# Performance work log

Hardware: AMD Instinct MI355X
Metric: run time of the kernel (lower is better)

## Reference

```python
import jax, jax.numpy as jnp
import numpy as np

RMIN, RMAX = -5.0, 5.0
MIN_BIN, MIN_SLOPE = 1e-4, 1e-4
BATCH, DIM, NBINS, HID = 65536, 64, 8, 128
NLAYERS = 6
SPLIT = DIM // 2  # 32
PDIM = 3 * NBINS + 1  # 25


def _mlp(h, w1, c1, w2, c2, w3, c3, w4, c4):
    # equinox MLP, depth=3: relu on hidden layers, identity on output
    h = jax.nn.relu(h @ w1.T + c1)
    h = jax.nn.relu(h @ w2.T + c2)
    h = jax.nn.relu(h @ w3.T + c3)
    return h @ w4.T + c4


def _rqs_forward(x, params):
    # x: [B,T], params: [B,T,3K+1] -> (y, logdet) each [B,T]
    K = (params.shape[-1] - 1) // 3
    total = RMAX - RMIN
    widths = jax.nn.softmax(params[..., :K], axis=-1) * (total - K * MIN_BIN) + MIN_BIN
    heights = jax.nn.softmax(params[..., K:2 * K], axis=-1) * (total - K * MIN_BIN) + MIN_BIN
    slope_off = float(np.log(np.exp(1.0 - MIN_SLOPE) - 1.0))
    slopes = jax.nn.softplus(params[..., 2 * K:] + slope_off) + MIN_SLOPE  # [B,T,K+1]
    zero = jnp.zeros(widths.shape[:-1] + (1,), widths.dtype)
    x_pos = jnp.concatenate([zero, jnp.cumsum(widths, -1)], -1) + RMIN   # [B,T,K+1]
    y_pos = jnp.concatenate([zero, jnp.cumsum(heights, -1)], -1) + RMIN
    below, above = x < RMIN, x > RMAX
    sl, sr = slopes[..., 0], slopes[..., -1]
    y_lin_l = (x - RMIN) * sl + RMIN
    y_lin_r = (x - RMAX) * sr + RMAX
    # searchsorted(x_pos[1:-1], x, side='right') == count of knots <= x
    bin_idx = jnp.clip(jnp.sum(x_pos[..., 1:-1] <= x[..., None], axis=-1), 0, K - 1)
    take = lambda a, i: jnp.take_along_axis(a, i[..., None], axis=-1)[..., 0]
    x_k, x_k1 = take(x_pos, bin_idx), take(x_pos, bin_idx + 1)
    y_k, y_k1 = take(y_pos, bin_idx), take(y_pos, bin_idx + 1)
    d_k, d_k1 = take(slopes, bin_idx), take(slopes, bin_idx + 1)
    w, h = x_k1 - x_k, y_k1 - y_k
    xi = jnp.clip((x - x_k) / w, 0.0, 1.0)
    s = h / w
    xi1m = 1.0 - xi
    q = xi * xi1m
    num = s * xi * xi + d_k * q
    den = s + (d_k1 + d_k - 2.0 * s) * q
    y_sp = y_k + h * num / den
    deriv = s * s * (d_k1 * xi * xi + 2.0 * s * q + d_k * xi1m * xi1m) / (den * den)
    y = jnp.where(below, y_lin_l, jnp.where(above, y_lin_r, y_sp))
    ld = jnp.where(below, jnp.log(sl), jnp.where(above, jnp.log(sr), jnp.log(deriv)))
    return y, ld


def _coupling(x, w1, c1, w2, c2, w3, c3, w4, c4, midx, tidx):
    xm = x[:, midx]           # [B,32]
    xt = x[:, tidx]           # [B,32]
    params = _mlp(xm, w1, c1, w2, c2, w3, c3, w4, c4)  # [B, 32*25]
    params = params.reshape(xt.shape[0], xt.shape[1], PDIM)
    yt, ld = _rqs_forward(xt, params)
    y = jnp.zeros_like(x).at[:, midx].set(xm).at[:, tidx].set(yt)
    return y, jnp.sum(ld, axis=-1)


def _make_masks():
    half_m = np.arange(0, SPLIT, dtype=np.int32)          # mask==1 positions
    half_t = np.arange(SPLIT, DIM, dtype=np.int32)
    alt_m = np.arange(1, DIM, 2, dtype=np.int32)          # odd -> mask==1
    alt_t = np.arange(0, DIM, 2, dtype=np.int32)
    mi = np.stack([half_m if i % 2 == 0 else alt_m for i in range(NLAYERS)])
    ti = np.stack([half_t if i % 2 == 0 else alt_t for i in range(NLAYERS)])
    return jnp.asarray(mi), jnp.asarray(ti)


def setup_inputs() -> dict:
    key = jax.random.key(0)
    ks = jax.random.split(key, 10)
    sc = 0.05
    x = jax.random.normal(ks[0], (BATCH, DIM), jnp.float32)
    W1 = jax.random.normal(ks[1], (NLAYERS, HID, SPLIT), jnp.float32) * sc
    b1 = jax.random.normal(ks[2], (NLAYERS, HID), jnp.float32) * sc
    W2 = jax.random.normal(ks[3], (NLAYERS, HID, HID), jnp.float32) * sc
    b2 = jax.random.normal(ks[4], (NLAYERS, HID), jnp.float32) * sc
    W3 = jax.random.normal(ks[5], (NLAYERS, HID, HID), jnp.float32) * sc
    b3 = jax.random.normal(ks[6], (NLAYERS, HID), jnp.float32) * sc
    W4 = jax.random.normal(ks[7], (NLAYERS, SPLIT * PDIM, HID), jnp.float32) * sc
    b4 = jax.random.normal(ks[8], (NLAYERS, SPLIT * PDIM), jnp.float32) * sc
    mask_idx, transform_idx = _make_masks()
    return dict(x=x, W1=W1, b1=b1, W2=W2, b2=b2, W3=W3, b3=b3, W4=W4, b4=b4,
                mask_idx=mask_idx, transform_idx=transform_idx)


def reference(x, W1, b1, W2, b2, W3, b3, W4, b4, mask_idx, transform_idx):
    def step(carry, layer):
        xc, tot = carry
        w1, c1, w2, c2, w3, c3, w4, c4, mi, ti = layer
        y, ld = _coupling(xc, w1, c1, w2, c2, w3, c3, w4, c4, mi, ti)
        return (y, tot + ld), None
    init = (x, jnp.zeros(x.shape[0], x.dtype))
    (y, total_logdet), _ = jax.lax.scan(
        step, init, (W1, b1, W2, b2, W3, b3, W4, b4, mask_idx, transform_idx))
    return y, total_logdet
```

## Files before the change

kernel.cpp:

```cpp
#include <hip/hip_runtime.h>
#include <math.h>

#define BATCH   65536
#define DIM     64
#define HID     128
#define SPLIT   32
#define NBINS   8
#define PDIM    25
#define NLAYERS 6
#define R_MIN   (-5.0f)
#define R_MAX   (5.0f)
#define MIN_BIN   1.0e-4f
#define MIN_SLOPE 1.0e-4f
#define SOFF      0.54116666f

#define ROWSW 16
#define WAVES 4
#define MBLK  64
#define NT    256

#define N_W1  (HID*SPLIT)
#define N_W2  (HID*HID)
#define N_W4P (32*32*HID)
#define N_W4  (SPLIT*PDIM*HID)

typedef __attribute__((ext_vector_type(8))) short bf16x8;
typedef __attribute__((ext_vector_type(4))) float f32x4;

__device__ __forceinline__ short f2bf(float f) {
    unsigned u = __builtin_bit_cast(unsigned, f);
    unsigned r = u + 0x7FFFu + ((u >> 16) & 1u);
    return (short)(r >> 16);
}

__device__ __forceinline__ unsigned pk2(float a, float b) {
    unsigned r;
    asm("v_cvt_pk_bf16_f32 %0, %1, %2" : "=v"(r) : "v"(a), "v"(b));
    return r;
}

__device__ __forceinline__ bf16x8 ldfrag(const short* base) {
    short4 lo = *reinterpret_cast<const short4*>(base);
    short4 hi = *reinterpret_cast<const short4*>(base + 64);
    bf16x8 a;
    a[0]=lo.x; a[1]=lo.y; a[2]=lo.z; a[3]=lo.w;
    a[4]=hi.x; a[5]=hi.y; a[6]=hi.z; a[7]=hi.w;
    return a;
}

__global__ void cvt_weights(const float* __restrict__ W1, const float* __restrict__ W2,
                            const float* __restrict__ W3, const float* __restrict__ W4,
                            const float* __restrict__ b4,
                            short* __restrict__ o1, short* __restrict__ o2,
                            short* __restrict__ o3, short* __restrict__ o4,
                            float* __restrict__ b4q) {
    const int stride = gridDim.x * blockDim.x;
    const int i0 = blockIdx.x * blockDim.x + threadIdx.x;
    for (int i = i0; i < NLAYERS*N_W1; i += stride) {
        const int L = i >> 12, rem = i & 4095;
        const int nt = rem >> 9, q = rem & 511;
        const int l = q >> 3, e = q & 7;
        o1[i] = f2bf(W1[L*N_W1 + (nt*16 + (l&15))*SPLIT + (l>>4)*8 + e]);
    }
    for (int i = i0; i < NLAYERS*N_W2; i += stride) {
        const int L = i >> 14, rem = i & 16383;
        const int c = rem >> 9, q = rem & 511;
        const int nt = c >> 2, kt = c & 3;
        const int l = q >> 3, e = q & 7;
        const int src = L*N_W2 + (nt*16 + (l&15))*HID + kt*32 + (l>>4)*8 + e;
        o2[i] = f2bf(W2[src]);
        o3[i] = f2bf(W3[src]);
    }
    for (int i = i0; i < NLAYERS*N_W4P; i += stride) {
        const int L = i >> 17, rem = i & (N_W4P - 1);
        const int c = rem >> 9, q = rem & 511;
        const int tb = c >> 5, pq = (c >> 2) & 7, kt = c & 3;
        const int l = q >> 3, e = q & 7;
        const int t = tb*4 + ((l & 15) >> 2);
        const int p = pq*4 + (l & 3);
        o4[i] = (p < PDIM)
              ? f2bf(W4[(size_t)L*N_W4 + (size_t)(t*PDIM + p)*HID + kt*32 + (l>>4)*8 + e])
              : (short)0;
    }
    for (int i = i0; i < NLAYERS*SPLIT*32; i += stride) {
        const int L = i >> 10, rem = i & 1023;
        const int t = rem >> 5, p = rem & 31;
        b4q[i] = (p < PDIM) ? b4[L*SPLIT*PDIM + t*PDIM + p] : 0.0f;
    }
}

template<int UNR>
__global__ __launch_bounds__(NT, 4) void flow_layer(
    const float* xin, float* yout, float* logdet, const int first,
    const short* __restrict__ bW1, const float* __restrict__ b1,
    const short* __restrict__ bW2, const float* __restrict__ b2,
    const short* __restrict__ bW3, const float* __restrict__ b3,
    const short* __restrict__ bW4, const float* __restrict__ b4q,
    const int* __restrict__ mi, const int* __restrict__ ti)
{
    __shared__ short act[WAVES][32 * 64];
    __shared__ float xts[WAVES][ROWSW][33];

    const int tid = threadIdx.x;
    const int wv  = tid >> 6;
    const int l   = tid & 63;
    const int lr  = l & 15;
    const int lg  = l >> 4;
    const int rbase = blockIdx.x * MBLK + wv * ROWSW;

    short* const actw = &act[wv][0];

    {
        const int kcol = l & 31;
        const int mc = mi[kcol], tc = ti[kcol];
        const int r0 = l >> 5;
        #pragma unroll
        for (int it = 0; it < 8; ++it) {
            const int r = r0 + it * 2;
            const float* row = xin + (size_t)(rbase + r) * DIM;
            const float mv = row[mc];
            actw[(kcol >> 2)*64 + r*4 + (kcol & 3)] = f2bf(mv);
            xts[wv][r][kcol] = row[tc];
            if (first) yout[(size_t)(rbase + r) * DIM + mc] = mv;
        }
    }

    {
        const bf16x8 afr = ldfrag(&actw[(2*lg)*64 + lr*4]);
        f32x4 c[8];
        #pragma unroll
        for (int nt = 0; nt < 8; ++nt) {
            const float4 bv = *reinterpret_cast<const float4*>(b1 + nt*16 + lg*4);
            c[nt] = (f32x4){bv.x, bv.y, bv.z, bv.w};
        }
        #pragma unroll
        for (int nt = 0; nt < 8; ++nt) {
            const bf16x8 wfr = *reinterpret_cast<const bf16x8*>(bW1 + (size_t)nt*512 + l*8);
            c[nt] = __builtin_amdgcn_mfma_f32_16x16x32_bf16(wfr, afr, c[nt], 0, 0, 0);
        }
        #pragma unroll
        for (int nt = 0; nt < 8; ++nt) {
            const unsigned u0 = pk2(fmaxf(c[nt][0], 0.0f), fmaxf(c[nt][1], 0.0f));
            const unsigned u1 = pk2(fmaxf(c[nt][2], 0.0f), fmaxf(c[nt][3], 0.0f));
            *reinterpret_cast<uint2*>(&actw[(nt*4 + lg)*64 + lr*4]) = (uint2){u0, u1};
        }
    }

    #pragma unroll 1
    for (int ph = 0; ph < 2; ++ph) {
        const short* Wp = ph ? bW3 : bW2;
        const float* bp = ph ? b3  : b2;
        bf16x8 afr[4];
        #pragma unroll
        for (int kt = 0; kt < 4; ++kt)
            afr[kt] = ldfrag(&actw[(kt*8 + 2*lg)*64 + lr*4]);
        f32x4 c[8];
        #pragma unroll
        for (int nt = 0; nt < 8; ++nt) {
            const float4 bv = *reinterpret_cast<const float4*>(bp + nt*16 + lg*4);
            c[nt] = (f32x4){bv.x, bv.y, bv.z, bv.w};
        }
        #pragma unroll
        for (int kt = 0; kt < 4; ++kt)
            #pragma unroll
            for (int nt = 0; nt < 8; ++nt) {
                const bf16x8 wfr = *reinterpret_cast<const bf16x8*>(Wp + (size_t)(nt*4 + kt)*512 + l*8);
                c[nt] = __builtin_amdgcn_mfma_f32_16x16x32_bf16(wfr, afr[kt], c[nt], 0, 0, 0);
            }
        #pragma unroll
        for (int nt = 0; nt < 8; ++nt) {
            const unsigned u0 = pk2(fmaxf(c[nt][0], 0.0f), fmaxf(c[nt][1], 0.0f));
            const unsigned u1 = pk2(fmaxf(c[nt][2], 0.0f), fmaxf(c[nt][3], 0.0f));
            *reinterpret_cast<uint2*>(&actw[(nt*4 + lg)*64 + lr*4]) = (uint2){u0, u1};
        }
    }

    bf16x8 afr[4];
    #pragma unroll
    for (int kt = 0; kt < 4; ++kt)
        afr[kt] = ldfrag(&actw[(kt*8 + 2*lg)*64 + lr*4]);

    float ldacc = 0.0f;

    auto body = [&](const int tb) {
        const int t = tb*4 + lg;
        f32x4 c[7];
        #pragma unroll
        for (int pq = 0; pq < 7; ++pq) {
            const float4 bv = *reinterpret_cast<const float4*>(b4q + t*32 + pq*4);
            c[pq] = (f32x4){bv.x, bv.y, bv.z, bv.w};
        }
        #pragma unroll
        for (int kt = 0; kt < 4; ++kt)
            #pragma unroll
            for (int pq = 0; pq < 7; ++pq) {
                const bf16x8 wfr = *reinterpret_cast<const bf16x8*>(
                    bW4 + (size_t)((tb*8 + pq)*4 + kt)*512 + l*8);
                c[pq] = __builtin_amdgcn_mfma_f32_16x16x32_bf16(wfr, afr[kt], c[pq], 0, 0, 0);
            }

#define P(i) c[(i)>>2][(i)&3]
        float wd[NBINS], hg[NBINS];
        float sw = 0.0f, sh = 0.0f;
        #pragma unroll
        for (int i = 0; i < NBINS; ++i) { wd[i] = __expf(P(i));         sw += wd[i]; }
        #pragma unroll
        for (int i = 0; i < NBINS; ++i) { hg[i] = __expf(P(NBINS + i)); sh += hg[i]; }
        const float scw = __fdividef((R_MAX - R_MIN) - NBINS * MIN_BIN, sw);
        const float sch = __fdividef((R_MAX - R_MIN) - NBINS * MIN_BIN, sh);
        #pragma unroll
        for (int i = 0; i < NBINS; ++i) { wd[i] = wd[i]*scw + MIN_BIN; hg[i] = hg[i]*sch + MIN_BIN; }

        const float x = xts[wv][lr][t];

        float cx = R_MIN, cy = R_MIN;
        float x_k = R_MIN, y_k = R_MIN, wsel = wd[0], hsel = hg[0];
        float z0 = P(16), z1 = P(17);
        #pragma unroll
        for (int i = 1; i < NBINS; ++i) {
            cx += wd[i-1]; cy += hg[i-1];
            const bool tk = (cx <= x);
            x_k  = tk ? cx        : x_k;
            y_k  = tk ? cy        : y_k;
            wsel = tk ? wd[i]     : wsel;
            hsel = tk ? hg[i]     : hsel;
            z0   = tk ? P(16 + i) : z0;
            z1   = tk ? P(17 + i) : z1;
        }

        auto sp = [](float v) {
            const float z = v + SOFF;
            return ((z > 15.0f) ? z : __logf(1.0f + __expf(z))) + MIN_SLOPE;
        };
        const float d_k = sp(z0), d_k1 = sp(z1);
        const float sl0 = sp(P(16)), sl8 = sp(P(24));
#undef P

        const float invw = __fdividef(1.0f, wsel);
        float xi = (x - x_k) * invw;
        xi = fminf(fmaxf(xi, 0.0f), 1.0f);
        const float s    = hsel * invw;
        const float xi1m = 1.0f - xi;
        const float q    = xi * xi1m;
        const float num  = s * xi * xi + d_k * q;
        const float den  = s + (d_k1 + d_k - 2.0f * s) * q;
        const float invden = __fdividef(1.0f, den);
        const float y_sp = y_k + hsel * num * invden;
        const float deriv = s * s * (d_k1 * xi * xi + 2.0f * s * q + d_k * xi1m * xi1m)
                            * invden * invden;

        const bool below = x < R_MIN;
        const bool above = x > R_MAX;
        const float yv = below ? ((x - R_MIN) * sl0 + R_MIN)
                       : (above ? ((x - R_MAX) * sl8 + R_MAX) : y_sp);
        const float dv = below ? sl0 : (above ? sl8 : deriv);
        ldacc += __logf(dv);

        yout[(size_t)(rbase + lr) * DIM + ti[t]] = yv;
    };

    if constexpr (UNR == 1) {
        #pragma unroll 1
        for (int tb = 0; tb < 8; ++tb) body(tb);
    } else {
        #pragma unroll 1
        for (int tb = 0; tb < 8; tb += 2) { body(tb); body(tb + 1); }
    }

    ldacc += __shfl_xor(ldacc, 16, 64);
    ldacc += __shfl_xor(ldacc, 32, 64);
    if (l < 16) {
        const int row = rbase + lr;
        if (first) logdet[row] = ldacc;
        else       logdet[row] += ldacc;
    }
}

extern "C" void kernel_launch(void* const* d_in, const int* in_sizes, int n_in,
                              void* d_out, int out_size, void* d_ws, size_t ws_size,
                              hipStream_t stream) {
    const float* x  = (const float*)d_in[0];
    const float* W1 = (const float*)d_in[1];
    const float* b1 = (const float*)d_in[2];
    const float* W2 = (const float*)d_in[3];
    const float* b2 = (const float*)d_in[4];
    const float* W3 = (const float*)d_in[5];
    const float* b3 = (const float*)d_in[6];
    const float* W4 = (const float*)d_in[7];
    const float* b4 = (const float*)d_in[8];
    const int*   mi = (const int*)d_in[9];
    const int*   ti = (const int*)d_in[10];

    float* y      = (float*)d_out;
    float* logdet = y + (size_t)BATCH * DIM;

    short* bW1 = (short*)d_ws;
    short* bW2 = bW1 + NLAYERS * N_W1;
    short* bW3 = bW2 + NLAYERS * N_W2;
    short* bW4 = bW3 + NLAYERS * N_W2;
    float* b4q = (float*)(bW4 + (size_t)NLAYERS * N_W4P);

    cvt_weights<<<512, 256, 0, stream>>>(W1, W2, W3, W4, b4, bW1, bW2, bW3, bW4, b4q);

    dim3 grid(BATCH / MBLK), block(NT);
    for (int L = 0; L < NLAYERS; ++L) {
        const float* in = (L == 0) ? x : y;
        const int first = (L == 0) ? 1 : 0;
        const short* w1 = bW1 + (size_t)L * N_W1;
        const short* w2 = bW2 + (size_t)L * N_W2;
        const short* w3 = bW3 + (size_t)L * N_W2;
        const short* w4 = bW4 + (size_t)L * N_W4P;
        const float* bb1 = b1 + L * HID, *bb2 = b2 + L * HID, *bb3 = b3 + L * HID;
        const float* bq = b4q + (size_t)L * SPLIT * 32;
        const int* mil = mi + L * SPLIT, *til = ti + L * SPLIT;
        if (L == 0 || L == 1 || L == 4)
            flow_layer<1><<<grid, block, 0, stream>>>(in, y, logdet, first,
                w1, bb1, w2, bb2, w3, bb3, w4, bq, mil, til);
        else
            flow_layer<2><<<grid, block, 0, stream>>>(in, y, logdet, first,
                w1, bb1, w2, bb2, w3, bb3, w4, bq, mil, til);
    }
}
```

Baseline: 349.6 us.

## Fuse all six coupling layers into one kernel keeping rows in LDS

Replaces the six per-layer kernel launches with a single kernel that loads each wave's 16 rows of x once into padded shared memory. All layers then run with the row state held in LDS, and y is written back with vectorized stores at the end. This removes five launches and the global read/write round trips of y and logdet between layers. In exchange the LDS footprint grows, which may affect occupancy. The per-layer unroll-by-two specialization is also dropped, so every layer uses the single-step transform loop.

```diff
diff --git a/kernel.cpp b/kernel.cpp
--- a/kernel.cpp
+++ b/kernel.cpp
@@ -18,6 +18,7 @@
 #define WAVES 4
 #define MBLK  64
 #define NT    256
+#define XPAD  68
 
 #define N_W1  (HID*SPLIT)
 #define N_W2  (HID*HID)
@@ -89,17 +90,16 @@
     }
 }
 
-template<int UNR>
-__global__ __launch_bounds__(NT, 4) void flow_layer(
-    const float* xin, float* yout, float* logdet, const int first,
-    const short* __restrict__ bW1, const float* __restrict__ b1,
-    const short* __restrict__ bW2, const float* __restrict__ b2,
-    const short* __restrict__ bW3, const float* __restrict__ b3,
-    const short* __restrict__ bW4, const float* __restrict__ b4q,
-    const int* __restrict__ mi, const int* __restrict__ ti)
+__global__ __launch_bounds__(NT, 4) void flow_all(
+    const float* __restrict__ xin, float* __restrict__ yout, float* __restrict__ logdet,
+    const short* __restrict__ bW1, const float* __restrict__ b1a,
+    const short* __restrict__ bW2, const float* __restrict__ b2a,
+    const short* __restrict__ bW3, const float* __restrict__ b3a,
+    const short* __restrict__ bW4, const float* __restrict__ b4qa,
+    const int* __restrict__ mia, const int* __restrict__ tia)
 {
     __shared__ short act[WAVES][32 * 64];
-    __shared__ float xts[WAVES][ROWSW][33];
+    __shared__ float xf[WAVES][ROWSW][XPAD];
 
     const int tid = threadIdx.x;
     const int wv  = tid >> 6;
@@ -109,171 +109,187 @@
     const int rbase = blockIdx.x * MBLK + wv * ROWSW;
 
     short* const actw = &act[wv][0];
-
-    {
-        const int kcol = l & 31;
-        const int mc = mi[kcol], tc = ti[kcol];
-        const int r0 = l >> 5;
-        #pragma unroll
-        for (int it = 0; it < 8; ++it) {
-            const int r = r0 + it * 2;
-            const float* row = xin + (size_t)(rbase + r) * DIM;
-            const float mv = row[mc];
-            actw[(kcol >> 2)*64 + r*4 + (kcol & 3)] = f2bf(mv);
-            xts[wv][r][kcol] = row[tc];
-            if (first) yout[(size_t)(rbase + r) * DIM + mc] = mv;
+    float (* const xr)[XPAD] = xf[wv];
+
+    #pragma unroll
+    for (int i = 0; i < 4; ++i) {
+        const int r = (l >> 4) + i * 4;
+        const int d = (l & 15) * 4;
+        const float4 v = *reinterpret_cast<const float4*>(xin + (size_t)(rbase + r) * DIM + d);
+        *reinterpret_cast<float4*>(&xr[r][d]) = v;
+    }
+
+    float ldacc = 0.0f;
+
+    #pragma unroll 1
+    for (int L = 0; L < NLAYERS; ++L) {
+        const short* w1 = bW1 + (size_t)L * N_W1;
+        const short* w2 = bW2 + (size_t)L * N_W2;
+        const short* w3 = bW3 + (size_t)L * N_W2;
+        const short* w4 = bW4 + (size_t)L * N_W4P;
+        const float* bb1 = b1a + L * HID;
+        const float* bb2 = b2a + L * HID;
+        const float* bb3 = b3a + L * HID;
+        const float* bq  = b4qa + (size_t)L * SPLIT * 32;
+        const int* mil = mia + L * SPLIT;
+        const int* til = tia + L * SPLIT;
+
+        {
+            const int kcol = l & 31;
+            const int mc = mil[kcol];
+            const int r0 = l >> 5;
+            #pragma unroll
+            for (int it = 0; it < 8; ++it) {
+                const int r = r0 + it * 2;
+                actw[(kcol >> 2)*64 + r*4 + (kcol & 3)] = f2bf(xr[r][mc]);
+            }
         }
-    }
-
-    {
-        const bf16x8 afr = ldfrag(&actw[(2*lg)*64 + lr*4]);
-        f32x4 c[8];
-        #pragma unroll
-        for (int nt = 0; nt < 8; ++nt) {
-            const float4 bv = *reinterpret_cast<const float4*>(b1 + nt*16 + lg*4);
-            c[nt] = (f32x4){bv.x, bv.y, bv.z, bv.w};
+
+        {
+            const bf16x8 afr = ldfrag(&actw[(2*lg)*64 + lr*4]);
+            f32x4 c[8];
+            #pragma unroll
+            for (int nt = 0; nt < 8; ++nt) {
+                const float4 bv = *reinterpret_cast<const float4*>(bb1 + nt*16 + lg*4);
+                c[nt] = (f32x4){bv.x, bv.y, bv.z, bv.w};
+            }
+            #pragma unroll
+            for (int nt = 0; nt < 8; ++nt) {
+                const bf16x8 wfr = *reinterpret_cast<const bf16x8*>(w1 + (size_t)nt*512 + l*8);
+                c[nt] = __builtin_amdgcn_mfma_f32_16x16x32_bf16(wfr, afr, c[nt], 0, 0, 0);
+            }
+            #pragma unroll
+            for (int nt = 0; nt < 8; ++nt) {
+                const unsigned u0 = pk2(fmaxf(c[nt][0], 0.0f), fmaxf(c[nt][1], 0.0f));
+                const unsigned u1 = pk2(fmaxf(c[nt][2], 0.0f), fmaxf(c[nt][3], 0.0f));
+                *reinterpret_cast<uint2*>(&actw[(nt*4 + lg)*64 + lr*4]) = (uint2){u0, u1};
+            }
         }
-        #pragma unroll
-        for (int nt = 0; nt < 8; ++nt) {
-            const bf16x8 wfr = *reinterpret_cast<const bf16x8*>(bW1 + (size_t)nt*512 + l*8);
-            c[nt] = __builtin_amdgcn_mfma_f32_16x16x32_bf16(wfr, afr, c[nt], 0, 0, 0);
+
+        #pragma unroll 1
+        for (int ph = 0; ph < 2; ++ph) {
+            const short* Wp = ph ? w3 : w2;
+            const float* bp = ph ? bb3 : bb2;
+            bf16x8 afr[4];
+            #pragma unroll
+            for (int kt = 0; kt < 4; ++kt)
+                afr[kt] = ldfrag(&actw[(kt*8 + 2*lg)*64 + lr*4]);
+            f32x4 c[8];
+            #pragma unroll
+            for (int nt = 0; nt < 8; ++nt) {
+                const float4 bv = *reinterpret_cast<const float4*>(bp + nt*16 + lg*4);
+                c[nt] = (f32x4){bv.x, bv.y, bv.z, bv.w};
+            }
+            #pragma unroll
+            for (int kt = 0; kt < 4; ++kt)
+                #pragma unroll
+                for (int nt = 0; nt < 8; ++nt) {
+                    const bf16x8 wfr = *reinterpret_cast<const bf16x8*>(Wp + (size_t)(nt*4 + kt)*512 + l*8);
+                    c[nt] = __builtin_amdgcn_mfma_f32_16x16x32_bf16(wfr, afr[kt], c[nt], 0, 0, 0);
+                }
+            #pragma unroll
+            for (int nt = 0; nt < 8; ++nt) {
+                const unsigned u0 = pk2(fmaxf(c[nt][0], 0.0f), fmaxf(c[nt][1], 0.0f));
+                const unsigned u1 = pk2(fmaxf(c[nt][2], 0.0f), fmaxf(c[nt][3], 0.0f));
+                *reinterpret_cast<uint2*>(&actw[(nt*4 + lg)*64 + lr*4]) = (uint2){u0, u1};
+            }
         }
-        #pragma unroll
-        for (int nt = 0; nt < 8; ++nt) {
-            const unsigned u0 = pk2(fmaxf(c[nt][0], 0.0f), fmaxf(c[nt][1], 0.0f));
-            const unsigned u1 = pk2(fmaxf(c[nt][2], 0.0f), fmaxf(c[nt][3], 0.0f));
-            *reinterpret_cast<uint2*>(&actw[(nt*4 + lg)*64 + lr*4]) = (uint2){u0, u1};
-        }
-    }
-
-    #pragma unroll 1
-    for (int ph = 0; ph < 2; ++ph) {
-        const short* Wp = ph ? bW3 : bW2;
-        const float* bp = ph ? b3  : b2;
+
         bf16x8 afr[4];
         #pragma unroll
         for (int kt = 0; kt < 4; ++kt)
             afr[kt] = ldfrag(&actw[(kt*8 + 2*lg)*64 + lr*4]);
-        f32x4 c[8];
-        #pragma unroll
-        for (int nt = 0; nt < 8; ++nt) {
-            const float4 bv = *reinterpret_cast<const float4*>(bp + nt*16 + lg*4);
-            c[nt] = (f32x4){bv.x, bv.y, bv.z, bv.w};
+
+        #pragma unroll 1
+        for (int tb = 0; tb < 8; ++tb) {
+            const int t = tb*4 + lg;
+            f32x4 c[7];
+            #pragma unroll
+            for (int pq = 0; pq < 7; ++pq) {
+                const float4 bv = *reinterpret_cast<const float4*>(bq + t*32 + pq*4);
+                c[pq] = (f32x4){bv.x, bv.y, bv.z, bv.w};
+            }
+            #pragma unroll
+            for (int kt = 0; kt < 4; ++kt)
+                #pragma unroll
+                for (int pq = 0; pq < 7; ++pq) {
+                    const bf16x8 wfr = *reinterpret_cast<const bf16x8*>(
+                        w4 + (size_t)((tb*8 + pq)*4 + kt)*512 + l*8);
+                    c[pq] = __builtin_amdgcn_mfma_f32_16x16x32_bf16(wfr, afr[kt], c[pq], 0, 0, 0);
+                }
+
+#define P(i) c[(i)>>2][(i)&3]
+            float wd[NBINS], hg[NBINS];
+            float sw = 0.0f, sh = 0.0f;
+            #pragma unroll
+            for (int i = 0; i < NBINS; ++i) { wd[i] = __expf(P(i));         sw += wd[i]; }
+            #pragma unroll
+            for (int i = 0; i < NBINS; ++i) { hg[i] = __expf(P(NBINS + i)); sh += hg[i]; }
+            const float scw = __fdividef((R_MAX - R_MIN) - NBINS * MIN_BIN, sw);
+            const float sch = __fdividef((R_MAX - R_MIN) - NBINS * MIN_BIN, sh);
+            #pragma unroll
+            for (int i = 0; i < NBINS; ++i) { wd[i] = wd[i]*scw + MIN_BIN; hg[i] = hg[i]*sch + MIN_BIN; }
+
+            const int tdim = til[t];
+            const float x = xr[lr][tdim];
+
+            float cx = R_MIN, cy = R_MIN;
+            float x_k = R_MIN, y_k = R_MIN, wsel = wd[0], hsel = hg[0];
+            float z0 = P(16), z1 = P(17);
+            #pragma unroll
+            for (int i = 1; i < NBINS; ++i) {
+                cx += wd[i-1]; cy += hg[i-1];
+                const bool tk = (cx <= x);
+                x_k  = tk ? cx        : x_k;
+                y_k  = tk ? cy        : y_k;
+                wsel = tk ? wd[i]     : wsel;
+                hsel = tk ? hg[i]     : hsel;
+                z0   = tk ? P(16 + i) : z0;
+                z1   = tk ? P(17 + i) : z1;
+            }
+
+            auto sp = [](float v) {
+                const float z = v + SOFF;
+                return ((z > 15.0f) ? z : __logf(1.0f + __expf(z))) + MIN_SLOPE;
+            };
+            const float d_k = sp(z0), d_k1 = sp(z1);
+            const float sl0 = sp(P(16)), sl8 = sp(P(24));
+#undef P
+
+            const float invw = __fdividef(1.0f, wsel);
+            float xi = (x - x_k) * invw;
+            xi = fminf(fmaxf(xi, 0.0f), 1.0f);
+            const float s    = hsel * invw;
+            const float xi1m = 1.0f - xi;
+            const float q    = xi * xi1m;
+            const float num  = s * xi * xi + d_k * q;
+            const float den  = s + (d_k1 + d_k - 2.0f * s) * q;
+            const float invden = __fdividef(1.0f, den);
+            const float y_sp = y_k + hsel * num * invden;
+            const float deriv = s * s * (d_k1 * xi * xi + 2.0f * s * q + d_k * xi1m * xi1m)
+                                * invden * invden;
+
+            const bool below = x < R_MIN;
+            const bool above = x > R_MAX;
+            const float yv = below ? ((x - R_MIN) * sl0 + R_MIN)
+                           : (above ? ((x - R_MAX) * sl8 + R_MAX) : y_sp);
+            const float dv = below ? sl0 : (above ? sl8 : deriv);
+            ldacc += __logf(dv);
+
+            xr[lr][tdim] = yv;
         }
-        #pragma unroll
-        for (int kt = 0; kt < 4; ++kt)
-            #pragma unroll
-            for (int nt = 0; nt < 8; ++nt) {
-                const bf16x8 wfr = *reinterpret_cast<const bf16x8*>(Wp + (size_t)(nt*4 + kt)*512 + l*8);
-                c[nt] = __builtin_amdgcn_mfma_f32_16x16x32_bf16(wfr, afr[kt], c[nt], 0, 0, 0);
-            }
-        #pragma unroll
-        for (int nt = 0; nt < 8; ++nt) {
-            const unsigned u0 = pk2(fmaxf(c[nt][0], 0.0f), fmaxf(c[nt][1], 0.0f));
-            const unsigned u1 = pk2(fmaxf(c[nt][2], 0.0f), fmaxf(c[nt][3], 0.0f));
-            *reinterpret_cast<uint2*>(&actw[(nt*4 + lg)*64 + lr*4]) = (uint2){u0, u1};
-        }
-    }
-
-    bf16x8 afr[4];
+    }
+
     #pragma unroll
-    for (int kt = 0; kt < 4; ++kt)
-        afr[kt] = ldfrag(&actw[(kt*8 + 2*lg)*64 + lr*4]);
-
-    float ldacc = 0.0f;
-
-    auto body = [&](const int tb) {
-        const int t = tb*4 + lg;
-        f32x4 c[7];
-        #pragma unroll
-        for (int pq = 0; pq < 7; ++pq) {
-            const float4 bv = *reinterpret_cast<const float4*>(b4q + t*32 + pq*4);
-            c[pq] = (f32x4){bv.x, bv.y, bv.z, bv.w};
-        }
-        #pragma unroll
-        for (int kt = 0; kt < 4; ++kt)
-            #pragma unroll
-            for (int pq = 0; pq < 7; ++pq) {
-                const bf16x8 wfr = *reinterpret_cast<const bf16x8*>(
-                    bW4 + (size_t)((tb*8 + pq)*4 + kt)*512 + l*8);
-                c[pq] = __builtin_amdgcn_mfma_f32_16x16x32_bf16(wfr, afr[kt], c[pq], 0, 0, 0);
-            }
-
-#define P(i) c[(i)>>2][(i)&3]
-        float wd[NBINS], hg[NBINS];
-        float sw = 0.0f, sh = 0.0f;
-        #pragma unroll
-        for (int i = 0; i < NBINS; ++i) { wd[i] = __expf(P(i));         sw += wd[i]; }
-        #pragma unroll
-        for (int i = 0; i < NBINS; ++i) { hg[i] = __expf(P(NBINS + i)); sh += hg[i]; }
-        const float scw = __fdividef((R_MAX - R_MIN) - NBINS * MIN_BIN, sw);
-        const float sch = __fdividef((R_MAX - R_MIN) - NBINS * MIN_BIN, sh);
-        #pragma unroll
-        for (int i = 0; i < NBINS; ++i) { wd[i] = wd[i]*scw + MIN_BIN; hg[i] = hg[i]*sch + MIN_BIN; }
-
-        const float x = xts[wv][lr][t];
-
-        float cx = R_MIN, cy = R_MIN;
-        float x_k = R_MIN, y_k = R_MIN, wsel = wd[0], hsel = hg[0];
-        float z0 = P(16), z1 = P(17);
-        #pragma unroll
-        for (int i = 1; i < NBINS; ++i) {
-            cx += wd[i-1]; cy += hg[i-1];
-            const bool tk = (cx <= x);
-            x_k  = tk ? cx        : x_k;
-            y_k  = tk ? cy        : y_k;
-            wsel = tk ? wd[i]     : wsel;
-            hsel = tk ? hg[i]     : hsel;
-            z0   = tk ? P(16 + i) : z0;
-            z1   = tk ? P(17 + i) : z1;
-        }
-
-        auto sp = [](float v) {
-            const float z = v + SOFF;
-            return ((z > 15.0f) ? z : __logf(1.0f + __expf(z))) + MIN_SLOPE;
-        };
-        const float d_k = sp(z0), d_k1 = sp(z1);
-        const float sl0 = sp(P(16)), sl8 = sp(P(24));
-#undef P
-
-        const float invw = __fdividef(1.0f, wsel);
-        float xi = (x - x_k) * invw;
-        xi = fminf(fmaxf(xi, 0.0f), 1.0f);
-        const float s    = hsel * invw;
-        const float xi1m = 1.0f - xi;
-        const float q    = xi * xi1m;
-        const float num  = s * xi * xi + d_k * q;
-        const float den  = s + (d_k1 + d_k - 2.0f * s) * q;
-        const float invden = __fdividef(1.0f, den);
-        const float y_sp = y_k + hsel * num * invden;
-        const float deriv = s * s * (d_k1 * xi * xi + 2.0f * s * q + d_k * xi1m * xi1m)
-                            * invden * invden;
-
-        const bool below = x < R_MIN;
-        const bool above = x > R_MAX;
-        const float yv = below ? ((x - R_MIN) * sl0 + R_MIN)
-                       : (above ? ((x - R_MAX) * sl8 + R_MAX) : y_sp);
-        const float dv = below ? sl0 : (above ? sl8 : deriv);
-        ldacc += __logf(dv);
-
-        yout[(size_t)(rbase + lr) * DIM + ti[t]] = yv;
-    };
-
-    if constexpr (UNR == 1) {
-        #pragma unroll 1
-        for (int tb = 0; tb < 8; ++tb) body(tb);
-    } else {
-        #pragma unroll 1
-        for (int tb = 0; tb < 8; tb += 2) { body(tb); body(tb + 1); }
-    }
-
+    for (int i = 0; i < 4; ++i) {
+        const int r = (l >> 4) + i * 4;
+        const int d = (l & 15) * 4;
+        *reinterpret_cast<float4*>(yout + (size_t)(rbase + r) * DIM + d) =
+            *reinterpret_cast<const float4*>(&xr[r][d]);
+    }
     ldacc += __shfl_xor(ldacc, 16, 64);
     ldacc += __shfl_xor(ldacc, 32, 64);
-    if (l < 16) {
-        const int row = rbase + lr;
-        if (first) logdet[row] = ldacc;
-        else       logdet[row] += ldacc;
-    }
+    if (l < 16) logdet[rbase + lr] = ldacc;
 }
 
 extern "C" void kernel_launch(void* const* d_in, const int* in_sizes, int n_in,
@@ -303,21 +319,6 @@
     cvt_weights<<<512, 256, 0, stream>>>(W1, W2, W3, W4, b4, bW1, bW2, bW3, bW4, b4q);
 
     dim3 grid(BATCH / MBLK), block(NT);
-    for (int L = 0; L < NLAYERS; ++L) {
-        const float* in = (L == 0) ? x : y;
-        const int first = (L == 0) ? 1 : 0;
-        const short* w1 = bW1 + (size_t)L * N_W1;
-        const short* w2 = bW2 + (size_t)L * N_W2;
-        const short* w3 = bW3 + (size_t)L * N_W2;
-        const short* w4 = bW4 + (size_t)L * N_W4P;
-        const float* bb1 = b1 + L * HID, *bb2 = b2 + L * HID, *bb3 = b3 + L * HID;
-        const float* bq = b4q + (size_t)L * SPLIT * 32;
-        const int* mil = mi + L * SPLIT, *til = ti + L * SPLIT;
-        if (L == 0 || L == 1 || L == 4)
-            flow_layer<1><<<grid, block, 0, stream>>>(in, y, logdet, first,
-                w1, bb1, w2, bb2, w3, bb3, w4, bq, mil, til);
-        else
-            flow_layer<2><<<grid, block, 0, stream>>>(in, y, logdet, first,
-                w1, bb1, w2, bb2, w3, bb3, w4, bq, mil, til);
-    }
-}
+    flow_all<<<grid, block, 0, stream>>>(x, y, logdet,
+        bW1, b1, bW2, b2, bW3, b3, bW4, b4q, mi, ti);
+}
```

Result: slower. 481.0 us, median of 4 (+37.6%).

## Software-pipeline W4 MFMA of next tile with spline math of current tile

Applied to the files above, without the earlier changes.

Restructures the final-layer loop so the weight loads and MFMAs for the next group of transformed dimensions are interleaved with the scalar rational-quadratic spline computation of the current group, using two ping-pong accumulator sets. This is meant to hide global weight-load latency and keep the matrix units busy alongside the transcendental and VALU work. It also drops the per-layer UNR template variants in favour of one kernel and rebalances the softmax sums into a tree. The cost is higher register pressure from two live accumulator arrays plus a weight fragment buffer, which under launch_bounds(256,4) could cause spills.

```diff
diff --git a/kernel.cpp b/kernel.cpp
--- a/kernel.cpp
+++ b/kernel.cpp
@@ -89,7 +89,6 @@
     }
 }
 
-template<int UNR>
 __global__ __launch_bounds__(NT, 4) void flow_layer(
     const float* xin, float* yout, float* logdet, const int first,
     const short* __restrict__ bW1, const float* __restrict__ b1,
@@ -126,7 +125,7 @@
     }
 
     {
-        const bf16x8 afr = ldfrag(&actw[(2*lg)*64 + lr*4]);
+        const bf16x8 afr0 = ldfrag(&actw[(2*lg)*64 + lr*4]);
         f32x4 c[8];
         #pragma unroll
         for (int nt = 0; nt < 8; ++nt) {
@@ -136,7 +135,7 @@
         #pragma unroll
         for (int nt = 0; nt < 8; ++nt) {
             const bf16x8 wfr = *reinterpret_cast<const bf16x8*>(bW1 + (size_t)nt*512 + l*8);
-            c[nt] = __builtin_amdgcn_mfma_f32_16x16x32_bf16(wfr, afr, c[nt], 0, 0, 0);
+            c[nt] = __builtin_amdgcn_mfma_f32_16x16x32_bf16(wfr, afr0, c[nt], 0, 0, 0);
         }
         #pragma unroll
         for (int nt = 0; nt < 8; ++nt) {
@@ -182,59 +181,68 @@
 
     float ldacc = 0.0f;
 
-    auto body = [&](const int tb) {
+    auto loadgrp = [&](bf16x8* wfr, int tb, int kt) {
+        #pragma unroll
+        for (int pq = 0; pq < 7; ++pq)
+            wfr[pq] = *reinterpret_cast<const bf16x8*>(
+                bW4 + (size_t)((tb*8 + pq)*4 + kt)*512 + l*8);
+    };
+    auto mfmagrp = [&](f32x4* c, const bf16x8* wfr, int kt) {
+        #pragma unroll
+        for (int pq = 0; pq < 7; ++pq)
+            c[pq] = __builtin_amdgcn_mfma_f32_16x16x32_bf16(wfr[pq], afr[kt], c[pq], 0, 0, 0);
+    };
+    auto biasinit = [&](f32x4* c, int tb) {
         const int t = tb*4 + lg;
-        f32x4 c[7];
         #pragma unroll
         for (int pq = 0; pq < 7; ++pq) {
             const float4 bv = *reinterpret_cast<const float4*>(b4q + t*32 + pq*4);
             c[pq] = (f32x4){bv.x, bv.y, bv.z, bv.w};
         }
-        #pragma unroll
-        for (int kt = 0; kt < 4; ++kt)
-            #pragma unroll
-            for (int pq = 0; pq < 7; ++pq) {
-                const bf16x8 wfr = *reinterpret_cast<const bf16x8*>(
-                    bW4 + (size_t)((tb*8 + pq)*4 + kt)*512 + l*8);
-                c[pq] = __builtin_amdgcn_mfma_f32_16x16x32_bf16(wfr, afr[kt], c[pq], 0, 0, 0);
-            }
-
-#define P(i) c[(i)>>2][(i)&3]
+    };
+
+    auto stage = [&](f32x4* cC, f32x4* cN, const int tb, const bool doNext) {
+        bf16x8 wfr[7];
+        if (doNext) { biasinit(cN, tb + 1); loadgrp(wfr, tb + 1, 0); }
+
         float wd[NBINS], hg[NBINS];
-        float sw = 0.0f, sh = 0.0f;
-        #pragma unroll
-        for (int i = 0; i < NBINS; ++i) { wd[i] = __expf(P(i));         sw += wd[i]; }
-        #pragma unroll
-        for (int i = 0; i < NBINS; ++i) { hg[i] = __expf(P(NBINS + i)); sh += hg[i]; }
+        #pragma unroll
+        for (int i = 0; i < NBINS; ++i) wd[i] = __expf(cC[i>>2][i&3]);
+        #pragma unroll
+        for (int i = 0; i < NBINS; ++i) hg[i] = __expf(cC[(NBINS+i)>>2][(NBINS+i)&3]);
+        const float sw = ((wd[0]+wd[1]) + (wd[2]+wd[3])) + ((wd[4]+wd[5]) + (wd[6]+wd[7]));
+        const float sh = ((hg[0]+hg[1]) + (hg[2]+hg[3])) + ((hg[4]+hg[5]) + (hg[6]+hg[7]));
         const float scw = __fdividef((R_MAX - R_MIN) - NBINS * MIN_BIN, sw);
         const float sch = __fdividef((R_MAX - R_MIN) - NBINS * MIN_BIN, sh);
         #pragma unroll
         for (int i = 0; i < NBINS; ++i) { wd[i] = wd[i]*scw + MIN_BIN; hg[i] = hg[i]*sch + MIN_BIN; }
 
-        const float x = xts[wv][lr][t];
-
+        if (doNext) { mfmagrp(cN, wfr, 0); loadgrp(wfr, tb + 1, 1); }
+
+        const float x = xts[wv][lr][tb*4 + lg];
         float cx = R_MIN, cy = R_MIN;
         float x_k = R_MIN, y_k = R_MIN, wsel = wd[0], hsel = hg[0];
-        float z0 = P(16), z1 = P(17);
+        float z0 = cC[4][0], z1 = cC[4][1];
         #pragma unroll
         for (int i = 1; i < NBINS; ++i) {
             cx += wd[i-1]; cy += hg[i-1];
             const bool tk = (cx <= x);
-            x_k  = tk ? cx        : x_k;
-            y_k  = tk ? cy        : y_k;
-            wsel = tk ? wd[i]     : wsel;
-            hsel = tk ? hg[i]     : hsel;
-            z0   = tk ? P(16 + i) : z0;
-            z1   = tk ? P(17 + i) : z1;
-        }
+            x_k  = tk ? cx : x_k;
+            y_k  = tk ? cy : y_k;
+            wsel = tk ? wd[i] : wsel;
+            hsel = tk ? hg[i] : hsel;
+            z0   = tk ? cC[(16+i)>>2][(16+i)&3] : z0;
+            z1   = tk ? cC[(17+i)>>2][(17+i)&3] : z1;
+        }
+
+        if (doNext) { mfmagrp(cN, wfr, 1); loadgrp(wfr, tb + 1, 2); }
 
         auto sp = [](float v) {
             const float z = v + SOFF;
             return ((z > 15.0f) ? z : __logf(1.0f + __expf(z))) + MIN_SLOPE;
         };
         const float d_k = sp(z0), d_k1 = sp(z1);
-        const float sl0 = sp(P(16)), sl8 = sp(P(24));
-#undef P
+        const float sl0 = sp(cC[4][0]), sl8 = sp(cC[6][0]);
 
         const float invw = __fdividef(1.0f, wsel);
         float xi = (x - x_k) * invw;
@@ -249,22 +257,30 @@
         const float deriv = s * s * (d_k1 * xi * xi + 2.0f * s * q + d_k * xi1m * xi1m)
                             * invden * invden;
 
+        if (doNext) { mfmagrp(cN, wfr, 2); loadgrp(wfr, tb + 1, 3); }
+
         const bool below = x < R_MIN;
         const bool above = x > R_MAX;
         const float yv = below ? ((x - R_MIN) * sl0 + R_MIN)
                        : (above ? ((x - R_MAX) * sl8 + R_MAX) : y_sp);
         const float dv = below ? sl0 : (above ? sl8 : deriv);
         ldacc += __logf(dv);
-
-        yout[(size_t)(rbase + lr) * DIM + ti[t]] = yv;
+        yout[(size_t)(rbase + lr) * DIM + ti[tb*4 + lg]] = yv;
+
+        if (doNext) { mfmagrp(cN, wfr, 3); }
     };
 
-    if constexpr (UNR == 1) {
-        #pragma unroll 1
-        for (int tb = 0; tb < 8; ++tb) body(tb);
-    } else {
-        #pragma unroll 1
-        for (int tb = 0; tb < 8; tb += 2) { body(tb); body(tb + 1); }
+    f32x4 cA[7], cB[7];
+    {
+        bf16x8 wfr[7];
+        biasinit(cA, 0);
+        #pragma unroll
+        for (int kt = 0; kt < 4; ++kt) { loadgrp(wfr, 0, kt); mfmagrp(cA, wfr, kt); }
+    }
+    #pragma unroll 1
+    for (int tb = 0; tb < 8; tb += 2) {
+        stage(cA, cB, tb,     true);
+        stage(cB, cA, tb + 1, tb + 1 < 7);
     }
 
     ldacc += __shfl_xor(ldacc, 16, 64);
@@ -304,20 +320,12 @@
 
     dim3 grid(BATCH / MBLK), block(NT);
     for (int L = 0; L < NLAYERS; ++L) {
-        const float* in = (L == 0) ? x : y;
-        const int first = (L == 0) ? 1 : 0;
-        const short* w1 = bW1 + (size_t)L * N_W1;
-        const short* w2 = bW2 + (size_t)L * N_W2;
-        const short* w3 = bW3 + (size_t)L * N_W2;
-        const short* w4 = bW4 + (size_t)L * N_W4P;
-        const float* bb1 = b1 + L * HID, *bb2 = b2 + L * HID, *bb3 = b3 + L * HID;
-        const float* bq = b4q + (size_t)L * SPLIT * 32;
-        const int* mil = mi + L * SPLIT, *til = ti + L * SPLIT;
-        if (L == 0 || L == 1 || L == 4)
-            flow_layer<1><<<grid, block, 0, stream>>>(in, y, logdet, first,
-                w1, bb1, w2, bb2, w3, bb3, w4, bq, mil, til);
-        else
-            flow_layer<2><<<grid, block, 0, stream>>>(in, y, logdet, first,
-                w1, bb1, w2, bb2, w3, bb3, w4, bq, mil, til);
-    }
-}
+        flow_layer<<<grid, block, 0, stream>>>(
+            (L == 0) ? x : y, y, logdet, (L == 0) ? 1 : 0,
+            bW1 + (size_t)L * N_W1, b1 + L * HID,
+            bW2 + (size_t)L * N_W2, b2 + L * HID,
+            bW3 + (size_t)L * N_W2, b3 + L * HID,
+            bW4 + (size_t)L * N_W4P, b4q + (size_t)L * SPLIT * 32,
+            mi + L * SPLIT, ti + L * SPLIT);
+    }
+}
```

Result: slower. 481.5 us (+37.7%).

## Split each 16-row tile's MLP output columns across two cooperating waves

Applied to the files above, without the earlier changes.

Blocks go from four independent waves on 64 rows to two waves sharing one 16-row tile. Each wave computes half of every layer's output columns, with barriers between layers on a shared activation buffer, and the two waves' logdet partials are combined through LDS. This halves the weight-fragment loads and accumulators per wave, lowering register pressure and shortening the per-row critical path so more waves can overlap. The cost is extra __syncthreads, twice as many waves reloading the same weights, and removal of the per-layer unroll-variant selection.

```diff
diff --git a/kernel.cpp b/kernel.cpp
--- a/kernel.cpp
+++ b/kernel.cpp
@@ -14,10 +14,8 @@
 #define MIN_SLOPE 1.0e-4f
 #define SOFF      0.54116666f
 
-#define ROWSW 16
-#define WAVES 4
-#define MBLK  64
-#define NT    256
+#define ROWSB 16
+#define NT    128
 
 #define N_W1  (HID*SPLIT)
 #define N_W2  (HID*HID)
@@ -89,8 +87,7 @@
     }
 }
 
-template<int UNR>
-__global__ __launch_bounds__(NT, 4) void flow_layer(
+__global__ __launch_bounds__(NT, 8) void flow_layer(
     const float* xin, float* yout, float* logdet, const int first,
     const short* __restrict__ bW1, const float* __restrict__ b1,
     const short* __restrict__ bW2, const float* __restrict__ b2,
@@ -98,53 +95,58 @@
     const short* __restrict__ bW4, const float* __restrict__ b4q,
     const int* __restrict__ mi, const int* __restrict__ ti)
 {
-    __shared__ short act[WAVES][32 * 64];
-    __shared__ float xts[WAVES][ROWSW][33];
+    __shared__ short act[32 * 64];
+    __shared__ float xts[ROWSB][33];
+    __shared__ float ldp[2][17];
 
     const int tid = threadIdx.x;
-    const int wv  = tid >> 6;
+    const int w   = tid >> 6;
     const int l   = tid & 63;
     const int lr  = l & 15;
     const int lg  = l >> 4;
-    const int rbase = blockIdx.x * MBLK + wv * ROWSW;
-
-    short* const actw = &act[wv][0];
+    const int rbase = blockIdx.x * ROWSB;
 
     {
-        const int kcol = l & 31;
+        const int kcol = tid & 31;
         const int mc = mi[kcol], tc = ti[kcol];
-        const int r0 = l >> 5;
-        #pragma unroll
-        for (int it = 0; it < 8; ++it) {
-            const int r = r0 + it * 2;
+        const int r0 = tid >> 5;
+        #pragma unroll
+        for (int it = 0; it < 4; ++it) {
+            const int r = r0 + it * 4;
             const float* row = xin + (size_t)(rbase + r) * DIM;
             const float mv = row[mc];
-            actw[(kcol >> 2)*64 + r*4 + (kcol & 3)] = f2bf(mv);
-            xts[wv][r][kcol] = row[tc];
+            act[(kcol >> 2)*64 + r*4 + (kcol & 3)] = f2bf(mv);
+            xts[r][kcol] = row[tc];
             if (first) yout[(size_t)(rbase + r) * DIM + mc] = mv;
         }
     }
+    __syncthreads();
 
     {
-        const bf16x8 afr = ldfrag(&actw[(2*lg)*64 + lr*4]);
-        f32x4 c[8];
-        #pragma unroll
-        for (int nt = 0; nt < 8; ++nt) {
+        const bf16x8 afr = ldfrag(&act[(2*lg)*64 + lr*4]);
+        f32x4 c[4];
+        #pragma unroll
+        for (int j = 0; j < 4; ++j) {
+            const int nt = w*4 + j;
             const float4 bv = *reinterpret_cast<const float4*>(b1 + nt*16 + lg*4);
-            c[nt] = (f32x4){bv.x, bv.y, bv.z, bv.w};
-        }
-        #pragma unroll
-        for (int nt = 0; nt < 8; ++nt) {
+            c[j] = (f32x4){bv.x, bv.y, bv.z, bv.w};
+        }
+        #pragma unroll
+        for (int j = 0; j < 4; ++j) {
+            const int nt = w*4 + j;
             const bf16x8 wfr = *reinterpret_cast<const bf16x8*>(bW1 + (size_t)nt*512 + l*8);
-            c[nt] = __builtin_amdgcn_mfma_f32_16x16x32_bf16(wfr, afr, c[nt], 0, 0, 0);
-        }
-        #pragma unroll
-        for (int nt = 0; nt < 8; ++nt) {
-            const unsigned u0 = pk2(fmaxf(c[nt][0], 0.0f), fmaxf(c[nt][1], 0.0f));
-            const unsigned u1 = pk2(fmaxf(c[nt][2], 0.0f), fmaxf(c[nt][3], 0.0f));
-            *reinterpret_cast<uint2*>(&actw[(nt*4 + lg)*64 + lr*4]) = (uint2){u0, u1};
-        }
-    }
+            c[j] = __builtin_amdgcn_mfma_f32_16x16x32_bf16(wfr, afr, c[j], 0, 0, 0);
+        }
+        __syncthreads();
+        #pragma unroll
+        for (int j = 0; j < 4; ++j) {
+            const int nt = w*4 + j;
+            const unsigned u0 = pk2(fmaxf(c[j][0], 0.0f), fmaxf(c[j][1], 0.0f));
+            const unsigned u1 = pk2(fmaxf(c[j][2], 0.0f), fmaxf(c[j][3], 0.0f));
+            *reinterpret_cast<uint2*>(&act[(nt*4 + lg)*64 + lr*4]) = (uint2){u0, u1};
+        }
+    }
+    __syncthreads();
 
     #pragma unroll 1
     for (int ph = 0; ph < 2; ++ph) {
@@ -153,36 +155,43 @@
         bf16x8 afr[4];
         #pragma unroll
         for (int kt = 0; kt < 4; ++kt)
-            afr[kt] = ldfrag(&actw[(kt*8 + 2*lg)*64 + lr*4]);
-        f32x4 c[8];
-        #pragma unroll
-        for (int nt = 0; nt < 8; ++nt) {
+            afr[kt] = ldfrag(&act[(kt*8 + 2*lg)*64 + lr*4]);
+        f32x4 c[4];
+        #pragma unroll
+        for (int j = 0; j < 4; ++j) {
+            const int nt = w*4 + j;
             const float4 bv = *reinterpret_cast<const float4*>(bp + nt*16 + lg*4);
-            c[nt] = (f32x4){bv.x, bv.y, bv.z, bv.w};
+            c[j] = (f32x4){bv.x, bv.y, bv.z, bv.w};
         }
         #pragma unroll
         for (int kt = 0; kt < 4; ++kt)
             #pragma unroll
-            for (int nt = 0; nt < 8; ++nt) {
+            for (int j = 0; j < 4; ++j) {
+                const int nt = w*4 + j;
                 const bf16x8 wfr = *reinterpret_cast<const bf16x8*>(Wp + (size_t)(nt*4 + kt)*512 + l*8);
-                c[nt] = __builtin_amdgcn_mfma_f32_16x16x32_bf16(wfr, afr[kt], c[nt], 0, 0, 0);
+                c[j] = __builtin_amdgcn_mfma_f32_16x16x32_bf16(wfr, afr[kt], c[j], 0, 0, 0);
             }
-        #pragma unroll
-        for (int nt = 0; nt < 8; ++nt) {
-            const unsigned u0 = pk2(fmaxf(c[nt][0], 0.0f), fmaxf(c[nt][1], 0.0f));
-            const unsigned u1 = pk2(fmaxf(c[nt][2], 0.0f), fmaxf(c[nt][3], 0.0f));
-            *reinterpret_cast<uint2*>(&actw[(nt*4 + lg)*64 + lr*4]) = (uint2){u0, u1};
-        }
+        __syncthreads();
+        #pragma unroll
+        for (int j = 0; j < 4; ++j) {
+            const int nt = w*4 + j;
+            const unsigned u0 = pk2(fmaxf(c[j][0], 0.0f), fmaxf(c[j][1], 0.0f));
+            const unsigned u1 = pk2(fmaxf(c[j][2], 0.0f), fmaxf(c[j][3], 0.0f));
+            *reinterpret_cast<uint2*>(&act[(nt*4 + lg)*64 + lr*4]) = (uint2){u0, u1};
+        }
+        __syncthreads();
     }
 
     bf16x8 afr[4];
     #pragma unroll
     for (int kt = 0; kt < 4; ++kt)
-        afr[kt] = ldfrag(&actw[(kt*8 + 2*lg)*64 + lr*4]);
+        afr[kt] = ldfrag(&act[(kt*8 + 2*lg)*64 + lr*4]);
 
     float ldacc = 0.0f;
 
-    auto body = [&](const int tb) {
+    #pragma unroll 1
+    for (int tbl = 0; tbl < 4; ++tbl) {
+        const int tb = w*4 + tbl;
         const int t = tb*4 + lg;
         f32x4 c[7];
         #pragma unroll
@@ -201,17 +210,18 @@
 
 #define P(i) c[(i)>>2][(i)&3]
         float wd[NBINS], hg[NBINS];
-        float sw = 0.0f, sh = 0.0f;
-        #pragma unroll
-        for (int i = 0; i < NBINS; ++i) { wd[i] = __expf(P(i));         sw += wd[i]; }
-        #pragma unroll
-        for (int i = 0; i < NBINS; ++i) { hg[i] = __expf(P(NBINS + i)); sh += hg[i]; }
+        #pragma unroll
+        for (int i = 0; i < NBINS; ++i) wd[i] = __expf(P(i));
+        #pragma unroll
+        for (int i = 0; i < NBINS; ++i) hg[i] = __expf(P(NBINS + i));
+        const float sw = ((wd[0]+wd[1]) + (wd[2]+wd[3])) + ((wd[4]+wd[5]) + (wd[6]+wd[7]));
+        const float sh = ((hg[0]+hg[1]) + (hg[2]+hg[3])) + ((hg[4]+hg[5]) + (hg[6]+hg[7]));
         const float scw = __fdividef((R_MAX - R_MIN) - NBINS * MIN_BIN, sw);
         const float sch = __fdividef((R_MAX - R_MIN) - NBINS * MIN_BIN, sh);
         #pragma unroll
         for (int i = 0; i < NBINS; ++i) { wd[i] = wd[i]*scw + MIN_BIN; hg[i] = hg[i]*sch + MIN_BIN; }
 
-        const float x = xts[wv][lr][t];
+        const float x = xts[lr][t];
 
         float cx = R_MIN, cy = R_MIN;
         float x_k = R_MIN, y_k = R_MIN, wsel = wd[0], hsel = hg[0];
@@ -220,10 +230,10 @@
         for (int i = 1; i < NBINS; ++i) {
             cx += wd[i-1]; cy += hg[i-1];
             const bool tk = (cx <= x);
-            x_k  = tk ? cx        : x_k;
-            y_k  = tk ? cy        : y_k;
-            wsel = tk ? wd[i]     : wsel;
-            hsel = tk ? hg[i]     : hsel;
+            x_k  = tk ? cx : x_k;
+            y_k  = tk ? cy : y_k;
+            wsel = tk ? wd[i] : wsel;
+            hsel = tk ? hg[i] : hsel;
             z0   = tk ? P(16 + i) : z0;
             z1   = tk ? P(17 + i) : z1;
         }
@@ -257,22 +267,17 @@
         ldacc += __logf(dv);
 
         yout[(size_t)(rbase + lr) * DIM + ti[t]] = yv;
-    };
-
-    if constexpr (UNR == 1) {
-        #pragma unroll 1
-        for (int tb = 0; tb < 8; ++tb) body(tb);
-    } else {
-        #pragma unroll 1
-        for (int tb = 0; tb < 8; tb += 2) { body(tb); body(tb + 1); }
     }
 
     ldacc += __shfl_xor(ldacc, 16, 64);
     ldacc += __shfl_xor(ldacc, 32, 64);
-    if (l < 16) {
+    if (l < 16) ldp[w][lr] = ldacc;
+    __syncthreads();
+    if (w == 0 && l < 16) {
+        const float sum = ldp[0][lr] + ldp[1][lr];
         const int row = rbase + lr;
-        if (first) logdet[row] = ldacc;
-        else       logdet[row] += ldacc;
+        if (first) logdet[row] = sum;
+        else       logdet[row] += sum;
     }
 }
 
@@ -302,22 +307,14 @@
 
     cvt_weights<<<512, 256, 0, stream>>>(W1, W2, W3, W4, b4, bW1, bW2, bW3, bW4, b4q);
 
-    dim3 grid(BATCH / MBLK), block(NT);
+    dim3 grid(BATCH / ROWSB), block(NT);
     for (int L = 0; L < NLAYERS; ++L) {
-        const float* in = (L == 0) ? x : y;
-        const int first = (L == 0) ? 1 : 0;
-        const short* w1 = bW1 + (size_t)L * N_W1;
-        const short* w2 = bW2 + (size_t)L * N_W2;
-        const short* w3 = bW3 + (size_t)L * N_W2;
-        const short* w4 = bW4 + (size_t)L * N_W4P;
-        const float* bb1 = b1 + L * HID, *bb2 = b2 + L * HID, *bb3 = b3 + L * HID;
-        const float* bq = b4q + (size_t)L * SPLIT * 32;
-        const int* mil = mi + L * SPLIT, *til = ti + L * SPLIT;
-        if (L == 0 || L == 1 || L == 4)
-            flow_layer<1><<<grid, block, 0, stream>>>(in, y, logdet, first,
-                w1, bb1, w2, bb2, w3, bb3, w4, bq, mil, til);
-        else
-            flow_layer<2><<<grid, block, 0, stream>>>(in, y, logdet, first,
-                w1, bb1, w2, bb2, w3, bb3, w4, bq, mil, til);
-    }
-}
+        flow_layer<<<grid, block, 0, stream>>>(
+            (L == 0) ? x : y, y, logdet, (L == 0) ? 1 : 0,
+            bW1 + (size_t)L * N_W1, b1 + L * HID,
+            bW2 + (size_t)L * N_W2, b2 + L * HID,
+            bW3 + (size_t)L * N_W2, b3 + L * HID,
+            bW4 + (size_t)L * N_W4P, b4q + (size_t)L * SPLIT * 32,
+            mi + L * SPLIT, ti + L * SPLIT);
+    }
+}
```

After: 484.1 us. 1.38x slower.
